# Kernel optimization log

Measured on AMD Instinct MI355X. Metric: run time of the kernel, lower is better.

## Reference

```python
import jax, jax.numpy as jnp
import numpy as np

TQ, TV, B, D, UNITS = 256, 1024, 4, 128, 128
NEG_INF = -1e9


def setup_inputs() -> dict:
    key = jax.random.key(0)
    k1, k2, k3, k4, k5, k6 = jax.random.split(key, 6)
    query = jax.random.normal(k1, (TQ, B, D), dtype=jnp.float32)
    value = jax.random.normal(k2, (TV, B, D), dtype=jnp.float32)
    mask = jax.random.randint(k3, (TV, B), 0, 2).astype(bool)
    # guarantee at least one valid key position per batch element
    mask = mask.at[0].set(True)
    # Dense kernels (glorot-uniform-like scaled normals are fine for a reference)
    W1 = jax.random.normal(k4, (D, UNITS), dtype=jnp.float32) * (1.0 / np.sqrt(D))
    W2 = jax.random.normal(k5, (D, UNITS), dtype=jnp.float32) * (1.0 / np.sqrt(D))
    # AdditiveAttention use_scale=True -> learnable scale vector of shape (units,)
    scale = jax.random.normal(k6, (UNITS,), dtype=jnp.float32) * (1.0 / np.sqrt(UNITS))
    return {"query": query, "value": value, "mask": mask, "W1": W1, "W2": W2, "scale": scale}


def reference(query, value, mask, W1, W2, scale):
    # time-major -> batch-major
    q = jnp.transpose(query, (1, 0, 2))   # [B, Tq, D]
    v = jnp.transpose(value, (1, 0, 2))   # [B, Tv, D]
    m = jnp.transpose(mask, (1, 0))       # [B, Tv] bool (value mask)

    wq = jnp.einsum('bqd,du->bqu', q, W1)  # [B, Tq, U]
    wk = jnp.einsum('bvd,du->bvu', v, W2)  # [B, Tv, U]

    # additive score: sum_u scale[u] * tanh(wq[b,q,u] + wk[b,v,u]) -> [B, Tq, Tv]
    scores = jnp.einsum('u,bqvu->bqv', scale, jnp.tanh(wq[:, :, None, :] + wk[:, None, :, :]))

    scores = jnp.where(m[:, None, :], scores, NEG_INF)
    attn = jax.nn.softmax(scores, axis=-1)          # [B, Tq, Tv]
    ctx = jnp.einsum('bqv,bvd->bqd', attn, v)       # [B, Tq, D]

    # batch-major -> time-major
    return jnp.transpose(ctx, (1, 0, 2))            # [Tq, B, D]
```

## Files before the change

kernel.cpp:

```cpp
#include <hip/hip_runtime.h>


#define TQ 256
#define TV 1024
#define BB 4
#define DD 128
#define UU 128
#define NEG_INF -1e9f
#define C2LOG2E 2.8853900817779268f

#define QUAD1(Av, Kv, sv, acc)                                     \
  { float d0 = __builtin_fmaf(Av.x, Kv.x, 1.f);                    \
    float d1 = __builtin_fmaf(Av.y, Kv.y, 1.f);                    \
    float d2 = __builtin_fmaf(Av.z, Kv.z, 1.f);                    \
    float d3 = __builtin_fmaf(Av.w, Kv.w, 1.f);                    \
    float m01 = d0 * d1, m23 = d2 * d3;                            \
    float R = __builtin_amdgcn_rcpf(m01 * m23);                    \
    float q01 = R * m23, q23 = R * m01;                            \
    acc = __builtin_fmaf(sv.x, q01 * d1, acc);                     \
    acc = __builtin_fmaf(sv.y, q01 * d0, acc);                     \
    acc = __builtin_fmaf(sv.z, q23 * d3, acc);                     \
    acc = __builtin_fmaf(sv.w, q23 * d2, acc); }

__global__ __launch_bounds__(256) void prep_kernel(
    const float* __restrict__ query, const float* __restrict__ value,
    const float* __restrict__ W1, const float* __restrict__ W2,
    const int* __restrict__ mask, const float* __restrict__ scale,
    float* __restrict__ Eq, float* __restrict__ Ek,
    int* __restrict__ valid_idx, int* __restrict__ nvalid,
    float* __restrict__ Ssum)
{
  __shared__ int   wsum[4];
  __shared__ float sred[2];
  const int t = threadIdx.x, lane = t & 63, wid = t >> 6;
  const int bid = blockIdx.x;

  if (bid < BB) {
    const int b = bid;
    int m[4];
#pragma unroll
    for (int k = 0; k < 4; ++k) m[k] = mask[(4 * t + k) * BB + b] ? 1 : 0;
    int cnt = m[0] + m[1] + m[2] + m[3];
    int pre = cnt;
#pragma unroll
    for (int off = 1; off < 64; off <<= 1) {
      int y = __shfl_up(pre, off, 64);
      if (lane >= off) pre += y;
    }
    if (lane == 63) wsum[wid] = pre;
    float sv_ = (t < UU) ? scale[t] : 0.f;
#pragma unroll
    for (int off = 32; off > 0; off >>= 1) sv_ += __shfl_xor(sv_, off, 64);
    if (t == 0)  sred[0] = sv_;
    if (t == 64) sred[1] = sv_;
    __syncthreads();
    int base = 0;
#pragma unroll
    for (int w = 0; w < 4; ++w) if (w < wid) base += wsum[w];
    int total = wsum[0] + wsum[1] + wsum[2] + wsum[3];
    int idx = base + pre - cnt;
#pragma unroll
    for (int k = 0; k < 4; ++k)
      if (m[k]) valid_idx[b * TV + (idx++)] = 4 * t + k;
    for (int i = t; i < TV; i += 256)
      if (i >= total) valid_idx[b * TV + i] = 0;
    if (t == 0) nvalid[b] = total;
    if (b == 0 && t == 0) Ssum[0] = sred[0] + sred[1];
  } else {
    const int R0 = (bid - BB) * 8;
    const bool isq = (R0 < TQ * BB);
    const float* X = isq ? query : value;
    const float* W = isq ? W1 : W2;
    float* E       = isq ? Eq : Ek;
    const int T    = isq ? TQ : TV;
    const int Rb   = isq ? R0 : (R0 - TQ * BB);
    const int uu_  = t & 127;
    const int half = t >> 7;
    const float* x0 = X + (size_t)(Rb + half * 4) * DD;
    float a0 = 0.f, a1 = 0.f, a2 = 0.f, a3 = 0.f;
#pragma unroll 8
    for (int d = 0; d < DD; ++d) {
      float wv = W[d * UU + uu_];
      a0 = __builtin_fmaf(x0[d], wv, a0);
      a1 = __builtin_fmaf(x0[DD + d], wv, a1);
      a2 = __builtin_fmaf(x0[2 * DD + d], wv, a2);
      a3 = __builtin_fmaf(x0[3 * DD + d], wv, a3);
    }
    float av[4] = {a0, a1, a2, a3};
#pragma unroll
    for (int i = 0; i < 4; ++i) {
      int rf = Rb + half * 4 + i;
      int b2 = rf & (BB - 1), tt = rf >> 2;
      E[((size_t)b2 * T + tt) * UU + uu_] =
          __builtin_amdgcn_exp2f(av[i] * C2LOG2E);
    }
  }
}

__global__ __launch_bounds__(512, 4) void attn_kernel(
    const float* __restrict__ value,
    const float* __restrict__ Eq,
    const float* __restrict__ Ek,
    const float* __restrict__ scale,
    const float* __restrict__ Ssum,
    const int*   __restrict__ valid_idx,
    const int*   __restrict__ nvalid,
    float* __restrict__ out)
{
  const int bid = blockIdx.x;
  const int b   = bid >> 7;
  const int q0  = (bid & 127) * 2;
  const int t   = threadIdx.x;
  const int lane = t & 63;

  __shared__ float4 kv[128 * 32];
  __shared__ float  s_lds[2][TV];
  __shared__ float4 eq_lds[2 * 32];
  __shared__ float4 sc_lds[32];
  __shared__ float  redm[2][4], reds[2][4], inv_s[2];
  __shared__ float  part[3][2][DD];

  const int nv  = nvalid[b];
  const int nvt = (nv + 127) >> 7;
  const float S = Ssum[0];

  if (t < 64) {
    int row = t >> 5, c = t & 31;
    eq_lds[row * 32 + (c ^ (c >> 3))] =
        ((const float4*)Eq)[((size_t)(b * TQ + q0 + row)) * 32 + c];
  } else if (t < 96) {
    int c = t & 31;
    sc_lds[c ^ (c >> 3)] = ((const float4*)scale)[c];
  }

  const int vl = t >> 2;
  const int uq = t & 3;
  const int sx = vl & 7;

  for (int tix = 0; tix < nvt; ++tix) {
    int rows[8];
    const int rb = b * TV + tix * 128 + (t >> 5);
#pragma unroll
    for (int k = 0; k < 8; ++k) rows[k] = valid_idx[rb + 16 * k];
    __syncthreads();
    {
      const float4* gk = (const float4*)Ek;
#pragma unroll
      for (int k = 0; k < 8; ++k) {
        int i = k * 512 + t;
        int r = i >> 5, c = i & 31;
        kv[r * 32 + (c ^ (r & 7))] = gk[((size_t)(b * TV + rows[k])) * 32 + c];
      }
    }
    __syncthreads();

    float acc0 = 0.f, acc1 = 0.f;
    const float4* Kr = kv + vl * 32;
#pragma unroll
    for (int j = 0; j < 8; ++j) {
      int uu = uq * 8 + j;
      float4 K  = Kr[uu ^ sx];
      int es = uu ^ uq;
      float4 A0 = eq_lds[es];
      float4 A1 = eq_lds[32 + es];
      float4 sv = sc_lds[es];
      QUAD1(A0, K, sv, acc0)
      QUAD1(A1, K, sv, acc1)
    }
    acc0 += __shfl_xor(acc0, 1, 64); acc0 += __shfl_xor(acc0, 2, 64);
    acc1 += __shfl_xor(acc1, 1, 64); acc1 += __shfl_xor(acc1, 2, 64);
    if (uq == 0) {
      s_lds[0][tix * 128 + vl] = __builtin_fmaf(-2.f, acc0, S);
      s_lds[1][tix * 128 + vl] = __builtin_fmaf(-2.f, acc1, S);
    }
  }
  __syncthreads();

  const int sq = t >> 8;
  const int si = t & 255;
  const int ws = (t >> 6) & 3;
  float xv[4];
  float mm = NEG_INF;
#pragma unroll
  for (int k = 0; k < 4; ++k) {
    int gv = si + 256 * k;
    xv[k] = (gv < nv) ? s_lds[sq][gv] : NEG_INF;
    mm = fmaxf(mm, xv[k]);
  }
#pragma unroll
  for (int off = 32; off > 0; off >>= 1)
    mm = fmaxf(mm, __shfl_xor(mm, off, 64));
  if (lane == 0) redm[sq][ws] = mm;
  __syncthreads();
  mm = fmaxf(fmaxf(redm[sq][0], redm[sq][1]), fmaxf(redm[sq][2], redm[sq][3]));

  float ssum = 0.f;
#pragma unroll
  for (int k = 0; k < 4; ++k) {
    float p = __expf(xv[k] - mm);
    s_lds[sq][si + 256 * k] = p;
    ssum += p;
  }
#pragma unroll
  for (int off = 32; off > 0; off >>= 1)
    ssum += __shfl_xor(ssum, off, 64);
  if (lane == 0) reds[sq][ws] = ssum;
  __syncthreads();
  if (t < 2)
    inv_s[t] = 1.f / (reds[t][0] + reds[t][1] + reds[t][2] + reds[t][3]);

  const int vq = t >> 7;
  const int dp = t & 127;
  float a0 = 0.f, a1 = 0.f;

  for (int tix = 0; tix < nvt; ++tix) {
    int rows[8];
    const int rb = b * TV + tix * 128 + (t >> 5);
#pragma unroll
    for (int k = 0; k < 8; ++k) rows[k] = valid_idx[rb + 16 * k];
    __syncthreads();
    {
      const float4* gv4 = (const float4*)value;
#pragma unroll
      for (int k = 0; k < 8; ++k) {
        int i = k * 512 + t;
        int r = i >> 5, c = i & 31;
        kv[r * 32 + c] = gv4[((size_t)rows[k] * BB + b) * 32 + c];
      }
    }
    __syncthreads();

    const float* Vf = (const float*)kv;
    const float4* p40 = (const float4*)&s_lds[0][tix * 128 + vq * 32];
    const float4* p41 = (const float4*)&s_lds[1][tix * 128 + vq * 32];
#pragma unroll
    for (int c8 = 0; c8 < 8; ++c8) {
      float4 p0 = p40[c8];
      float4 p1 = p41[c8];
      const float* Vr = Vf + (vq * 32 + c8 * 4) * 128 + dp;
      float v0 = Vr[0], v1 = Vr[128], v2 = Vr[256], v3 = Vr[384];
      a0 = __builtin_fmaf(p0.x, v0, a0); a1 = __builtin_fmaf(p1.x, v0, a1);
      a0 = __builtin_fmaf(p0.y, v1, a0); a1 = __builtin_fmaf(p1.y, v1, a1);
      a0 = __builtin_fmaf(p0.z, v2, a0); a1 = __builtin_fmaf(p1.z, v2, a1);
      a0 = __builtin_fmaf(p0.w, v3, a0); a1 = __builtin_fmaf(p1.w, v3, a1);
    }
  }

  if (vq) { part[vq - 1][0][dp] = a0; part[vq - 1][1][dp] = a1; }
  __syncthreads();
  if (vq == 0) {
    float o0 = a0 + part[0][0][dp] + part[1][0][dp] + part[2][0][dp];
    float o1 = a1 + part[0][1][dp] + part[1][1][dp] + part[2][1][dp];
    out[((size_t)q0 * BB + b) * DD + dp]       = o0 * inv_s[0];
    out[((size_t)(q0 + 1) * BB + b) * DD + dp] = o1 * inv_s[1];
  }
}

extern "C" void kernel_launch(void* const* d_in, const int* in_sizes, int n_in,
                              void* d_out, int out_size, void* d_ws, size_t ws_size,
                              hipStream_t stream) {
  const float* query = (const float*)d_in[0];
  const float* value = (const float*)d_in[1];
  const int*   mask  = (const int*)  d_in[2];
  const float* W1    = (const float*)d_in[3];
  const float* W2    = (const float*)d_in[4];
  const float* scale = (const float*)d_in[5];
  float* out = (float*)d_out;

  float* Eq      = (float*)d_ws;
  float* Ek      = Eq + (size_t)BB * TQ * UU;
  int*   vidx    = (int*)(Ek + (size_t)BB * TV * UU);
  int*   nvalid  = vidx + BB * TV;
  float* Ssum    = (float*)(nvalid + BB);

  prep_kernel<<<BB + (TQ + TV) * BB / 8, 256, 0, stream>>>(
      query, value, W1, W2, mask, scale, Eq, Ek, vidx, nvalid, Ssum);
  attn_kernel<<<BB * TQ / 2, 512, 0, stream>>>(
      value, Eq, Ek, scale, Ssum, vidx, nvalid, out);
}
```

Baseline: 51.03 us.

## Split attention over query and key tiles with static softmax bound and atomic reduction

Replaces the per-query-pair attention kernel with a grid of 16-query by 64-key tiles. Each tile computes scores, exponentiates against a fixed upper bound derived from the negative scale entries instead of a running max, and accumulates partial context and sums. The last tile per query group, found through an atomic counter, reduces the partials and normalizes. This raises reuse of Ek and value loads across queries and exposes more parallelism, at the cost of a global partial-buffer round trip and possible underflow if scores sit far below the static bound.

```diff
diff --git a/kernel.cpp b/kernel.cpp
--- a/kernel.cpp
+++ b/kernel.cpp
@@ -6,10 +6,11 @@
 #define BB 4
 #define DD 128
 #define UU 128
-#define NEG_INF -1e9f
+#define QTILES 16
+#define VTILES 16
 #define C2LOG2E 2.8853900817779268f
 
-#define QUAD1(Av, Kv, sv, acc)                                     \
+#define QUAD(Av, Kv, sv, acc)                                      \
   { float d0 = __builtin_fmaf(Av.x, Kv.x, 1.f);                    \
     float d1 = __builtin_fmaf(Av.y, Kv.y, 1.f);                    \
     float d2 = __builtin_fmaf(Av.z, Kv.z, 1.f);                    \
@@ -28,7 +29,7 @@
     const int* __restrict__ mask, const float* __restrict__ scale,
     float* __restrict__ Eq, float* __restrict__ Ek,
     int* __restrict__ valid_idx, int* __restrict__ nvalid,
-    float* __restrict__ Ssum)
+    float* __restrict__ SMp, int* __restrict__ cnt)
 {
   __shared__ int   wsum[4];
   __shared__ float sred[2];
@@ -37,11 +38,12 @@
 
   if (bid < BB) {
     const int b = bid;
+    if (bid == 0 && t < BB * QTILES) cnt[t] = 0;
     int m[4];
 #pragma unroll
     for (int k = 0; k < 4; ++k) m[k] = mask[(4 * t + k) * BB + b] ? 1 : 0;
-    int cnt = m[0] + m[1] + m[2] + m[3];
-    int pre = cnt;
+    int cntv = m[0] + m[1] + m[2] + m[3];
+    int pre = cntv;
 #pragma unroll
     for (int off = 1; off < 64; off <<= 1) {
       int y = __shfl_up(pre, off, 64);
@@ -49,23 +51,24 @@
     }
     if (lane == 63) wsum[wid] = pre;
     float sv_ = (t < UU) ? scale[t] : 0.f;
-#pragma unroll
-    for (int off = 32; off > 0; off >>= 1) sv_ += __shfl_xor(sv_, off, 64);
-    if (t == 0)  sred[0] = sv_;
-    if (t == 64) sred[1] = sv_;
+    float ng = fmaxf(-sv_, 0.f);
+#pragma unroll
+    for (int off = 32; off > 0; off >>= 1) ng += __shfl_xor(ng, off, 64);
+    if (t == 0)  sred[0] = ng;
+    if (t == 64) sred[1] = ng;
     __syncthreads();
     int base = 0;
 #pragma unroll
     for (int w = 0; w < 4; ++w) if (w < wid) base += wsum[w];
     int total = wsum[0] + wsum[1] + wsum[2] + wsum[3];
-    int idx = base + pre - cnt;
+    int idx = base + pre - cntv;
 #pragma unroll
     for (int k = 0; k < 4; ++k)
       if (m[k]) valid_idx[b * TV + (idx++)] = 4 * t + k;
     for (int i = t; i < TV; i += 256)
       if (i >= total) valid_idx[b * TV + i] = 0;
     if (t == 0) nvalid[b] = total;
-    if (b == 0 && t == 0) Ssum[0] = sred[0] + sred[1];
+    if (b == 0 && t == 0) SMp[0] = -2.f * (sred[0] + sred[1]);
   } else {
     const int R0 = (bid - BB) * 8;
     const bool isq = (R0 < TQ * BB);
@@ -97,162 +100,160 @@
   }
 }
 
-__global__ __launch_bounds__(512, 4) void attn_kernel(
+__global__ __launch_bounds__(256, 3) void partial_kernel(
     const float* __restrict__ value,
     const float* __restrict__ Eq,
     const float* __restrict__ Ek,
     const float* __restrict__ scale,
-    const float* __restrict__ Ssum,
+    const float* __restrict__ SMp,
     const int*   __restrict__ valid_idx,
     const int*   __restrict__ nvalid,
+    float* __restrict__ pctx,
+    float* __restrict__ psum,
+    int*   __restrict__ cnt,
     float* __restrict__ out)
 {
-  const int bid = blockIdx.x;
-  const int b   = bid >> 7;
-  const int q0  = (bid & 127) * 2;
-  const int t   = threadIdx.x;
-  const int lane = t & 63;
-
-  __shared__ float4 kv[128 * 32];
-  __shared__ float  s_lds[2][TV];
-  __shared__ float4 eq_lds[2 * 32];
-  __shared__ float4 sc_lds[32];
-  __shared__ float  redm[2][4], reds[2][4], inv_s[2];
-  __shared__ float  part[3][2][DD];
-
-  const int nv  = nvalid[b];
-  const int nvt = (nv + 127) >> 7;
-  const float S = Ssum[0];
-
-  if (t < 64) {
-    int row = t >> 5, c = t & 31;
-    eq_lds[row * 32 + (c ^ (c >> 3))] =
-        ((const float4*)Eq)[((size_t)(b * TQ + q0 + row)) * 32 + c];
-  } else if (t < 96) {
-    int c = t & 31;
-    sc_lds[c ^ (c >> 3)] = ((const float4*)scale)[c];
-  }
-
-  const int vl = t >> 2;
-  const int uq = t & 3;
-  const int sx = vl & 7;
-
-  for (int tix = 0; tix < nvt; ++tix) {
-    int rows[8];
-    const int rb = b * TV + tix * 128 + (t >> 5);
-#pragma unroll
-    for (int k = 0; k < 8; ++k) rows[k] = valid_idx[rb + 16 * k];
-    __syncthreads();
-    {
-      const float4* gk = (const float4*)Ek;
-#pragma unroll
-      for (int k = 0; k < 8; ++k) {
-        int i = k * 512 + t;
-        int r = i >> 5, c = i & 31;
-        kv[r * 32 + (c ^ (r & 7))] = gk[((size_t)(b * TV + rows[k])) * 32 + c];
+  const int vt = blockIdx.x, qt = blockIdx.y, b = blockIdx.z;
+  const int q0 = qt * 16, v0 = vt * 64;
+  const int t = threadIdx.x;
+  const int nv = nvalid[b];
+  const float SM = SMp[0];
+
+  __shared__ float4 ek_lds[64 * 32];
+  __shared__ float4 eq_lds[16 * 32];
+  __shared__ float  pT[64][16];
+  __shared__ int    oldv_sh;
+
+  {
+    const float4* gq = (const float4*)Eq + ((size_t)(b * TQ + q0)) * 32;
+    eq_lds[t]       = gq[t];
+    eq_lds[256 + t] = gq[256 + t];
+  }
+  {
+    const float4* gk = (const float4*)Ek;
+#pragma unroll
+    for (int k = 0; k < 8; ++k) {
+      int i = k * 256 + t;
+      int r = i >> 5, c = i & 31;
+      int vrow = valid_idx[b * TV + v0 + r];
+      ek_lds[r * 32 + (c ^ (r & 7))] = gk[((size_t)(b * TV + vrow)) * 32 + c];
+    }
+  }
+  __syncthreads();
+
+  const int qp = t >> 5;
+  const int vp = t & 31;
+  const int sx = vp & 7;
+  const float4* Ar0 = eq_lds + (2 * qp) * 32;
+  const float4* Ar1 = Ar0 + 32;
+  const float4* Kr0 = ek_lds + vp * 32;
+  const float4* Kr1 = ek_lds + (vp + 32) * 32;
+  const float4* S4  = (const float4*)scale;
+
+  float a00 = 0.f, a01 = 0.f, a10 = 0.f, a11 = 0.f;
+#pragma unroll 8
+  for (int uu = 0; uu < 32; ++uu) {
+    float4 A0 = Ar0[uu];
+    float4 A1 = Ar1[uu];
+    int cs = uu ^ sx;
+    float4 K0 = Kr0[cs];
+    float4 K1 = Kr1[cs];
+    float4 sv = S4[uu];
+    QUAD(A0, K0, sv, a00)
+    QUAD(A0, K1, sv, a01)
+    QUAD(A1, K0, sv, a10)
+    QUAD(A1, K1, sv, a11)
+  }
+  const bool vok0 = (v0 + vp) < nv;
+  const bool vok1 = (v0 + vp + 32) < nv;
+  float p00 = vok0 ? __expf(__builtin_fmaf(-2.f, a00, SM)) : 0.f;
+  float p01 = vok1 ? __expf(__builtin_fmaf(-2.f, a01, SM)) : 0.f;
+  float p10 = vok0 ? __expf(__builtin_fmaf(-2.f, a10, SM)) : 0.f;
+  float p11 = vok1 ? __expf(__builtin_fmaf(-2.f, a11, SM)) : 0.f;
+
+  float r0 = p00 + p01, r1 = p10 + p11;
+#pragma unroll
+  for (int off = 1; off < 32; off <<= 1) {
+    r0 += __shfl_xor(r0, off, 64);
+    r1 += __shfl_xor(r1, off, 64);
+  }
+  const size_t gidx = (size_t)(b * QTILES + qt) * VTILES + vt;
+  if (vp == 0) {
+    psum[gidx * 16 + 2 * qp]     = r0;
+    psum[gidx * 16 + 2 * qp + 1] = r1;
+  }
+
+  pT[vp][2 * qp]          = p00;
+  pT[vp + 32][2 * qp]     = p01;
+  pT[vp][2 * qp + 1]      = p10;
+  pT[vp + 32][2 * qp + 1] = p11;
+  __syncthreads();
+
+  const int vh = t >> 7;
+  const int d  = t & 127;
+  float acc[16];
+#pragma unroll
+  for (int j = 0; j < 16; ++j) acc[j] = 0.f;
+
+  const int ibase = vh * 32;
+  for (int i = ibase; i < ibase + 32; ++i) {
+    int vrow = valid_idx[b * TV + v0 + i];
+    float vv = value[((size_t)vrow * BB + b) * DD + d];
+    float4 pa0 = *((const float4*)&pT[i][0]);
+    float4 pa1 = *((const float4*)&pT[i][4]);
+    float4 pa2 = *((const float4*)&pT[i][8]);
+    float4 pa3 = *((const float4*)&pT[i][12]);
+    acc[0]  = __builtin_fmaf(pa0.x, vv, acc[0]);
+    acc[1]  = __builtin_fmaf(pa0.y, vv, acc[1]);
+    acc[2]  = __builtin_fmaf(pa0.z, vv, acc[2]);
+    acc[3]  = __builtin_fmaf(pa0.w, vv, acc[3]);
+    acc[4]  = __builtin_fmaf(pa1.x, vv, acc[4]);
+    acc[5]  = __builtin_fmaf(pa1.y, vv, acc[5]);
+    acc[6]  = __builtin_fmaf(pa1.z, vv, acc[6]);
+    acc[7]  = __builtin_fmaf(pa1.w, vv, acc[7]);
+    acc[8]  = __builtin_fmaf(pa2.x, vv, acc[8]);
+    acc[9]  = __builtin_fmaf(pa2.y, vv, acc[9]);
+    acc[10] = __builtin_fmaf(pa2.z, vv, acc[10]);
+    acc[11] = __builtin_fmaf(pa2.w, vv, acc[11]);
+    acc[12] = __builtin_fmaf(pa3.x, vv, acc[12]);
+    acc[13] = __builtin_fmaf(pa3.y, vv, acc[13]);
+    acc[14] = __builtin_fmaf(pa3.z, vv, acc[14]);
+    acc[15] = __builtin_fmaf(pa3.w, vv, acc[15]);
+  }
+
+  float* part = (float*)ek_lds;
+  if (vh == 1) {
+#pragma unroll
+    for (int j = 0; j < 16; ++j) part[j * 128 + d] = acc[j];
+  }
+  __syncthreads();
+  if (vh == 0) {
+    float* dst = pctx + gidx * (16 * 128);
+#pragma unroll
+    for (int j = 0; j < 16; ++j)
+      dst[j * 128 + d] = acc[j] + part[j * 128 + d];
+  }
+
+  __syncthreads();
+  __threadfence();
+  if (t == 0)
+    oldv_sh = __hip_atomic_fetch_add(&cnt[b * QTILES + qt], 1,
+                                     __ATOMIC_ACQ_REL, __HIP_MEMORY_SCOPE_AGENT);
+  __syncthreads();
+  if (oldv_sh == VTILES - 1) {
+    __threadfence();
+    const int dc = t & 127, qg = t >> 7;
+    const size_t gbase = (size_t)(b * QTILES + qt) * VTILES;
+#pragma unroll
+    for (int j = 0; j < 8; ++j) {
+      int q = qg * 8 + j;
+      float tot = 0.f, s = 0.f;
+      for (int v2 = 0; v2 < VTILES; ++v2) {
+        tot += pctx[(gbase + v2) * (16 * 128) + q * 128 + dc];
+        s   += psum[(gbase + v2) * 16 + q];
       }
-    }
-    __syncthreads();
-
-    float acc0 = 0.f, acc1 = 0.f;
-    const float4* Kr = kv + vl * 32;
-#pragma unroll
-    for (int j = 0; j < 8; ++j) {
-      int uu = uq * 8 + j;
-      float4 K  = Kr[uu ^ sx];
-      int es = uu ^ uq;
-      float4 A0 = eq_lds[es];
-      float4 A1 = eq_lds[32 + es];
-      float4 sv = sc_lds[es];
-      QUAD1(A0, K, sv, acc0)
-      QUAD1(A1, K, sv, acc1)
-    }
-    acc0 += __shfl_xor(acc0, 1, 64); acc0 += __shfl_xor(acc0, 2, 64);
-    acc1 += __shfl_xor(acc1, 1, 64); acc1 += __shfl_xor(acc1, 2, 64);
-    if (uq == 0) {
-      s_lds[0][tix * 128 + vl] = __builtin_fmaf(-2.f, acc0, S);
-      s_lds[1][tix * 128 + vl] = __builtin_fmaf(-2.f, acc1, S);
-    }
-  }
-  __syncthreads();
-
-  const int sq = t >> 8;
-  const int si = t & 255;
-  const int ws = (t >> 6) & 3;
-  float xv[4];
-  float mm = NEG_INF;
-#pragma unroll
-  for (int k = 0; k < 4; ++k) {
-    int gv = si + 256 * k;
-    xv[k] = (gv < nv) ? s_lds[sq][gv] : NEG_INF;
-    mm = fmaxf(mm, xv[k]);
-  }
-#pragma unroll
-  for (int off = 32; off > 0; off >>= 1)
-    mm = fmaxf(mm, __shfl_xor(mm, off, 64));
-  if (lane == 0) redm[sq][ws] = mm;
-  __syncthreads();
-  mm = fmaxf(fmaxf(redm[sq][0], redm[sq][1]), fmaxf(redm[sq][2], redm[sq][3]));
-
-  float ssum = 0.f;
-#pragma unroll
-  for (int k = 0; k < 4; ++k) {
-    float p = __expf(xv[k] - mm);
-    s_lds[sq][si + 256 * k] = p;
-    ssum += p;
-  }
-#pragma unroll
-  for (int off = 32; off > 0; off >>= 1)
-    ssum += __shfl_xor(ssum, off, 64);
-  if (lane == 0) reds[sq][ws] = ssum;
-  __syncthreads();
-  if (t < 2)
-    inv_s[t] = 1.f / (reds[t][0] + reds[t][1] + reds[t][2] + reds[t][3]);
-
-  const int vq = t >> 7;
-  const int dp = t & 127;
-  float a0 = 0.f, a1 = 0.f;
-
-  for (int tix = 0; tix < nvt; ++tix) {
-    int rows[8];
-    const int rb = b * TV + tix * 128 + (t >> 5);
-#pragma unroll
-    for (int k = 0; k < 8; ++k) rows[k] = valid_idx[rb + 16 * k];
-    __syncthreads();
-    {
-      const float4* gv4 = (const float4*)value;
-#pragma unroll
-      for (int k = 0; k < 8; ++k) {
-        int i = k * 512 + t;
-        int r = i >> 5, c = i & 31;
-        kv[r * 32 + c] = gv4[((size_t)rows[k] * BB + b) * 32 + c];
-      }
-    }
-    __syncthreads();
-
-    const float* Vf = (const float*)kv;
-    const float4* p40 = (const float4*)&s_lds[0][tix * 128 + vq * 32];
-    const float4* p41 = (const float4*)&s_lds[1][tix * 128 + vq * 32];
-#pragma unroll
-    for (int c8 = 0; c8 < 8; ++c8) {
-      float4 p0 = p40[c8];
-      float4 p1 = p41[c8];
-      const float* Vr = Vf + (vq * 32 + c8 * 4) * 128 + dp;
-      float v0 = Vr[0], v1 = Vr[128], v2 = Vr[256], v3 = Vr[384];
-      a0 = __builtin_fmaf(p0.x, v0, a0); a1 = __builtin_fmaf(p1.x, v0, a1);
-      a0 = __builtin_fmaf(p0.y, v1, a0); a1 = __builtin_fmaf(p1.y, v1, a1);
-      a0 = __builtin_fmaf(p0.z, v2, a0); a1 = __builtin_fmaf(p1.z, v2, a1);
-      a0 = __builtin_fmaf(p0.w, v3, a0); a1 = __builtin_fmaf(p1.w, v3, a1);
-    }
-  }
-
-  if (vq) { part[vq - 1][0][dp] = a0; part[vq - 1][1][dp] = a1; }
-  __syncthreads();
-  if (vq == 0) {
-    float o0 = a0 + part[0][0][dp] + part[1][0][dp] + part[2][0][dp];
-    float o1 = a1 + part[0][1][dp] + part[1][1][dp] + part[2][1][dp];
-    out[((size_t)q0 * BB + b) * DD + dp]       = o0 * inv_s[0];
-    out[((size_t)(q0 + 1) * BB + b) * DD + dp] = o1 * inv_s[1];
+      out[((size_t)(q0 + q) * BB + b) * DD + dc] = tot * __builtin_amdgcn_rcpf(s);
+    }
   }
 }
 
@@ -267,14 +268,17 @@
   const float* scale = (const float*)d_in[5];
   float* out = (float*)d_out;
 
-  float* Eq      = (float*)d_ws;
-  float* Ek      = Eq + (size_t)BB * TQ * UU;
-  int*   vidx    = (int*)(Ek + (size_t)BB * TV * UU);
-  int*   nvalid  = vidx + BB * TV;
-  float* Ssum    = (float*)(nvalid + BB);
+  float* Eq     = (float*)d_ws;
+  float* Ek     = Eq + (size_t)BB * TQ * UU;
+  float* pctx   = Ek + (size_t)BB * TV * UU;
+  float* psum   = pctx + (size_t)BB * QTILES * VTILES * 16 * 128;
+  float* SMp    = psum + (size_t)BB * QTILES * VTILES * 16;
+  int*   vidx   = (int*)(SMp + 1);
+  int*   nvalid = vidx + BB * TV;
+  int*   cnt    = nvalid + BB;
 
   prep_kernel<<<BB + (TQ + TV) * BB / 8, 256, 0, stream>>>(
-      query, value, W1, W2, mask, scale, Eq, Ek, vidx, nvalid, Ssum);
-  attn_kernel<<<BB * TQ / 2, 512, 0, stream>>>(
-      value, Eq, Ek, scale, Ssum, vidx, nvalid, out);
+      query, value, W1, W2, mask, scale, Eq, Ek, vidx, nvalid, SMp, cnt);
+  partial_kernel<<<dim3(VTILES, QTILES, BB), 256, 0, stream>>>(
+      value, Eq, Ek, scale, SMp, vidx, nvalid, pctx, psum, cnt, out);
 }
```

Result: slower. 195.3 us (+282.6%).
